# Kernel tuning notes

Hardware: AMD Instinct MI355X
Metric: run time of the kernel (lower is better)

## Reference

```python
import jax, jax.numpy as jnp
import numpy as np

B, S, D, H, E, K, V, FF, P = 1, 2048, 1024, 16, 8, 2, 32000, 4096, 4096
HD = D // H
EPS = 1e-5


def setup_inputs() -> dict:
    key = jax.random.key(0)
    ks = iter(jax.random.split(key, 64))
    w = lambda shape: jax.random.normal(next(ks), shape, jnp.float32) * 0.02
    d = {}
    d['input_ids'] = jax.random.randint(next(ks), (B, S), 0, V)
    d['embed_w'] = w((V, D))
    d['pos_w'] = w((P, D))
    for i in (0, 1):
        d[f'b{i}_ln1_g'] = jnp.ones(D); d[f'b{i}_ln1_b'] = jnp.zeros(D)
        d[f'b{i}_in_w'] = w((3 * D, D)); d[f'b{i}_in_b'] = jnp.zeros(3 * D)
        d[f'b{i}_out_w'] = w((D, D)); d[f'b{i}_out_b'] = jnp.zeros(D)
        d[f'b{i}_ln2_g'] = jnp.ones(D); d[f'b{i}_ln2_b'] = jnp.zeros(D)
    d['b0_ffn_w1'] = w((FF, D)); d['b0_ffn_b1'] = jnp.zeros(FF)
    d['b0_ffn_w2'] = w((D, FF)); d['b0_ffn_b2'] = jnp.zeros(D)
    d['b1_gate_w'] = w((E, D)); d['b1_gate_b'] = jnp.zeros(E)
    d['b1_moe_w1'] = w((E, FF, D)); d['b1_moe_b1'] = jnp.zeros((E, FF))
    d['b1_moe_w2'] = w((E, D, FF)); d['b1_moe_b2'] = jnp.zeros((E, D))
    d['norm_g'] = jnp.ones(D); d['norm_b'] = jnp.zeros(D)
    d['head_w'] = w((V, D))
    return d


def _ln(x, g, b):
    m = jnp.mean(x, -1, keepdims=True)
    v = jnp.mean(jnp.square(x - m), -1, keepdims=True)
    return (x - m) * jax.lax.rsqrt(v + EPS) * g + b


def _mha(x, in_w, in_b, out_w, out_b):
    # torch nn.MultiheadAttention (batch_first, eval mode -> no dropout)
    qkv = x @ in_w.T + in_b  # [B,S,3D]
    q, k, v = jnp.split(qkv, 3, axis=-1)
    q = q.reshape(B, S, H, HD); k = k.reshape(B, S, H, HD); v = v.reshape(B, S, H, HD)
    scores = jnp.einsum('bqhd,bkhd->bhqk', q, k) / jnp.sqrt(jnp.float32(HD))
    attn = jax.nn.softmax(scores, axis=-1)
    o = jnp.einsum('bhqk,bkhd->bqhd', attn, v).reshape(B, S, D)
    return o @ out_w.T + out_b


def _moe(h, gate_w, gate_b, w1, b1, w2, b2):
    scores = h @ gate_w.T + gate_b                       # [B,S,E]
    top_s, top_i = jax.lax.top_k(scores, K)              # [B,S,K]
    weights = jax.nn.softmax(top_s, axis=-1)             # softmax over top-k
    onehot = jax.nn.one_hot(top_i, E, dtype=h.dtype)     # [B,S,K,E]
    combine = jnp.sum(onehot * weights[..., None], axis=-2)  # [B,S,E]
    hid = jax.nn.gelu(jnp.einsum('bsd,efd->bsef', h, w1) + b1, approximate=False)
    eo = jnp.einsum('bsef,edf->bsed', hid, w2) + b2      # [B,S,E,D]
    return jnp.einsum('bsed,bse->bsd', eo, combine)


def reference(input_ids, embed_w, pos_w,
              b0_ln1_g, b0_ln1_b, b0_in_w, b0_in_b, b0_out_w, b0_out_b, b0_ln2_g, b0_ln2_b,
              b0_ffn_w1, b0_ffn_b1, b0_ffn_w2, b0_ffn_b2,
              b1_ln1_g, b1_ln1_b, b1_in_w, b1_in_b, b1_out_w, b1_out_b, b1_ln2_g, b1_ln2_b,
              b1_gate_w, b1_gate_b, b1_moe_w1, b1_moe_b1, b1_moe_w2, b1_moe_b2,
              norm_g, norm_b, head_w):
    pos = jnp.arange(S)[None, :]
    x = jnp.take(embed_w, input_ids, axis=0) + jnp.take(pos_w, pos, axis=0)
    # block 0: dense FFN
    x = x + _mha(_ln(x, b0_ln1_g, b0_ln1_b), b0_in_w, b0_in_b, b0_out_w, b0_out_b)
    h = _ln(x, b0_ln2_g, b0_ln2_b)
    ffn = jax.nn.gelu(h @ b0_ffn_w1.T + b0_ffn_b1, approximate=False) @ b0_ffn_w2.T + b0_ffn_b2
    x = x + ffn  # integration layer assumed residual add
    # block 1: MoE
    x = x + _mha(_ln(x, b1_ln1_g, b1_ln1_b), b1_in_w, b1_in_b, b1_out_w, b1_out_b)
    h = _ln(x, b1_ln2_g, b1_ln2_b)
    x = x + _moe(h, b1_gate_w, b1_gate_b, b1_moe_w1, b1_moe_b1, b1_moe_w2, b1_moe_b2)
    x = _ln(x, norm_g, norm_b)
    return x @ head_w.T
```

## Files before the change

kernel.cpp:

```cpp
#include <hip/hip_runtime.h>
#include <hip/hip_bf16.h>
#include <math.h>

typedef unsigned short ushort_t;
typedef __attribute__((ext_vector_type(8))) __bf16 bf16x8;
typedef __attribute__((ext_vector_type(4))) float f32x4;
typedef __attribute__((ext_vector_type(8))) short s8v;
typedef __attribute__((ext_vector_type(4))) short s4v;

#define SQ 2048
#define DM 1024
#define NH 16
#define HDIM 64
#define FFD 4096
#define NVOC 32000

__device__ inline float b2f(unsigned short u) {
  union { unsigned int i; float f; } x; x.i = ((unsigned int)u) << 16; return x.f;
}
__device__ inline unsigned short f2b(float f) {
  __hip_bfloat16 h = __float2bfloat16(f);
  return *reinterpret_cast<unsigned short*>(&h);
}
__device__ inline void split2(float x, ushort_t& h, ushort_t& l) {
  h = f2b(x);
  l = f2b(x - b2f(h));
}
__device__ inline float geluf(float v) {
  return 0.5f * v * (1.0f + erff(v * 0.70710678118654752f));
}
__device__ __forceinline__ void gld16(const void* g, void* l) {
  __builtin_amdgcn_global_load_lds(
      (const __attribute__((address_space(1))) void*)g,
      (__attribute__((address_space(3))) void*)l, 16, 0, 0);
}
#define MFMA __builtin_amdgcn_mfma_f32_16x16x32_bf16

template<int EPI, int NT, int KS>
__device__ __forceinline__ void gemmsp_body(
    const ushort_t* __restrict__ AH, const ushort_t* __restrict__ AL,
    int lda, long long bA,
    const ushort_t* __restrict__ BH, const ushort_t* __restrict__ BL,
    int ldb, long long bB,
    float* __restrict__ C, ushort_t* __restrict__ CH, ushort_t* __restrict__ CL,
    int ldc, long long bC, long long pC,
    int M, int N, int K, const float* __restrict__ bias, float alpha)
{
  int z = blockIdx.z, h = z / KS, kc = z % KS;
  const ushort_t* AHp = AH + (long long)h * bA + (long long)kc * K;
  const ushort_t* ALp = AL + (long long)h * bA + (long long)kc * K;
  const ushort_t* BHp = BH + (long long)h * bB + (long long)kc * K;
  const ushort_t* BLp = BL + (long long)h * bB + (long long)kc * K;
  int m0 = blockIdx.x * 128, n0 = blockIdx.y * NT;
  const int NF = NT / 32;

  __shared__ __align__(16) ushort_t sAH[128 * 32], sAL[128 * 32];
  __shared__ __align__(16) ushort_t sBH[NT * 32],  sBL[NT * 32];

  int tid = threadIdx.x, lane = tid & 63, wave = tid >> 6;
  int wr = (wave >> 1) * 64, wc = (wave & 1) * (NT >> 1);
  int l15 = lane & 15, l4 = lane >> 4;

  f32x4 acc[4][NF];
#pragma unroll
  for (int m = 0; m < 4; ++m)
#pragma unroll
    for (int n = 0; n < NF; ++n) acc[m][n] = (f32x4){0.f, 0.f, 0.f, 0.f};

  for (int k0 = 0; k0 < K; k0 += 32) {
#pragma unroll
    for (int i = 0; i < 2; ++i) {
      int fi = i * 2048 + tid * 8;
      int r = fi >> 5, chk = (fi >> 3) & 3;
      int scol = ((chk ^ ((r >> 1) & 3)) << 3);
      int ra = m0 + r; if (ra > M - 1) ra = M - 1;
      long long go = (long long)ra * lda + k0 + scol;
      gld16(AHp + go, &sAH[fi]);
      gld16(ALp + go, &sAL[fi]);
    }
#pragma unroll
    for (int i = 0; i < NT / 64; ++i) {
      int fi = i * 2048 + tid * 8;
      int r = fi >> 5, chk = (fi >> 3) & 3;
      int scol = ((chk ^ ((r >> 1) & 3)) << 3);
      int rb = n0 + r; if (rb > N - 1) rb = N - 1;
      long long go = (long long)rb * ldb + k0 + scol;
      gld16(BHp + go, &sBH[fi]);
      gld16(BLp + go, &sBL[fi]);
    }
    __syncthreads();
    bf16x8 ah[4], al[4], bh[NF], bl[NF];
#pragma unroll
    for (int m = 0; m < 4; ++m) {
      int r = wr + m * 16 + l15;
      int o = r * 32 + ((l4 ^ ((r >> 1) & 3)) << 3);
      ah[m] = *(const bf16x8*)&sAH[o];
      al[m] = *(const bf16x8*)&sAL[o];
    }
#pragma unroll
    for (int n = 0; n < NF; ++n) {
      int r = wc + n * 16 + l15;
      int o = r * 32 + ((l4 ^ ((r >> 1) & 3)) << 3);
      bh[n] = *(const bf16x8*)&sBH[o];
      bl[n] = *(const bf16x8*)&sBL[o];
    }
#pragma unroll
    for (int m = 0; m < 4; ++m)
#pragma unroll
      for (int n = 0; n < NF; ++n) {
        acc[m][n] = MFMA(ah[m], bh[n], acc[m][n], 0, 0, 0);
        acc[m][n] = MFMA(al[m], bh[n], acc[m][n], 0, 0, 0);
        acc[m][n] = MFMA(ah[m], bl[n], acc[m][n], 0, 0, 0);
      }
    __syncthreads();
  }

#pragma unroll
  for (int m = 0; m < 4; ++m) {
#pragma unroll
    for (int n = 0; n < NF; ++n) {
      int c = n0 + wc + n * 16 + l15;
      if (c >= N) continue;
      float bv = (EPI == 0 || EPI == 3 || EPI == 4) ? bias[c] : 0.f;
#pragma unroll
      for (int q = 0; q < 4; ++q) {
        int rr = m0 + wr + m * 16 + l4 * 4 + q;
        if (rr >= M) continue;
        float v = acc[m][n][q];
        if (EPI == 0) {
          ushort_t hh, ll; split2(v + bv, hh, ll);
          long long o = (long long)rr * ldc + c; CH[o] = hh; CL[o] = ll;
        } else if (EPI == 2) {
          C[(long long)kc * pC + (long long)rr * ldc + (long long)h * bC + c] = v;
        } else if (EPI == 3) {
          C[(long long)rr * ldc + c] += v + bv;
        } else if (EPI == 4) {
          ushort_t hh, ll; split2(geluf(v + bv), hh, ll);
          long long o = (long long)rr * ldc + c; CH[o] = hh; CL[o] = ll;
        }
      }
    }
  }
}

#define SP_ARGS const ushort_t* AH, const ushort_t* AL, int lda, long long bA, \
    const ushort_t* BH, const ushort_t* BL, int ldb, long long bB, \
    float* C, ushort_t* CH, ushort_t* CL, int ldc, long long bC, long long pC, \
    int M, int N, int K, const float* bias, float alpha
#define SP_PASS AH, AL, lda, bA, BH, BL, ldb, bB, C, CH, CL, ldc, bC, pC, M, N, K, bias, alpha

__global__ __launch_bounds__(256) void k_qkv (SP_ARGS) { gemmsp_body<0,128,1>(SP_PASS); }
__global__ __launch_bounds__(256) void k_outp(SP_ARGS) { gemmsp_body<2, 64,4>(SP_PASS); }
__global__ __launch_bounds__(256) void k_ffn1(SP_ARGS) { gemmsp_body<4,128,1>(SP_PASS); }
__global__ __launch_bounds__(256) void k_ffn2(SP_ARGS) { gemmsp_body<2, 64,2>(SP_PASS); }

template<int NP>
__global__ __launch_bounds__(256)
void reduce_add(float* __restrict__ x, const float* __restrict__ P, long long pC,
                const float* __restrict__ bias)
{
  int row = blockIdx.x, tid = threadIdx.x;
  long long o = (long long)row * DM + tid * 4;
  float4 xv = *(float4*)(x + o);
  float4 bv = *(const float4*)(bias + tid * 4);
  float sx = bv.x, sy = bv.y, sz = bv.z, sw = bv.w;
#pragma unroll
  for (int p = 0; p < NP; ++p) {
    float4 v = *(const float4*)(P + (long long)p * pC + o);
    sx += v.x; sy += v.y; sz += v.z; sw += v.w;
  }
  xv.x += sx; xv.y += sy; xv.z += sz; xv.w += sw;
  *(float4*)(x + o) = xv;
}

__global__ __launch_bounds__(256)
void k_attn(const ushort_t* __restrict__ qkvH, const ushort_t* __restrict__ qkvL,
            const ushort_t* __restrict__ VtH, const ushort_t* __restrict__ VtL,
            ushort_t* __restrict__ aH, ushort_t* __restrict__ aL)
{
  int f = blockIdx.x + blockIdx.y * gridDim.x;
  int logical = (f & 7) * 64 + (f >> 3);
  int q0 = (logical & 31) * 64;
  int h  = logical >> 5;

  __shared__ __align__(16) ushort_t sKH[4096], sKL[4096];
  __shared__ __align__(16) ushort_t sVH[4096], sVL[4096];
  __shared__ __align__(16) ushort_t sPH[4096], sPL[4096];

  int tid = threadIdx.x, lane = tid & 63, wave = tid >> 6;
  int l15 = lane & 15, l4 = lane >> 4;

  bf16x8 qh[2], ql[2];
  {
    long long base = (long long)(q0 + wave * 16 + l15) * (3 * DM) + h * 64 + l4 * 8;
    qh[0] = *(const bf16x8*)(qkvH + base);
    qh[1] = *(const bf16x8*)(qkvH + base + 32);
    ql[0] = *(const bf16x8*)(qkvL + base);
    ql[1] = *(const bf16x8*)(qkvL + base + 32);
  }

  float mrow[4], lrow[4];
  f32x4 Oacc[4];
#pragma unroll
  for (int r = 0; r < 4; ++r) { mrow[r] = -1e30f; lrow[r] = 0.f; }
#pragma unroll
  for (int n = 0; n < 4; ++n) Oacc[n] = (f32x4){0.f, 0.f, 0.f, 0.f};

  for (int kt = 0; kt < SQ / 64; ++kt) {
#pragma unroll
    for (int i = 0; i < 2; ++i) {
      int idx = i * 2048 + tid * 8;
      int row = idx >> 6, chk = (idx >> 3) & 7;
      int scol = ((chk ^ (row & 7)) << 3);
      long long gk = (long long)(kt * 64 + row) * (3 * DM) + DM + h * 64 + scol;
      long long gv = (long long)(h * 64 + row) * SQ + kt * 64 + scol;
      gld16(qkvH + gk, &sKH[idx]);
      gld16(qkvL + gk, &sKL[idx]);
      gld16(VtH + gv, &sVH[idx]);
      gld16(VtL + gv, &sVL[idx]);
    }
    __syncthreads();

    f32x4 S[4];
#pragma unroll
    for (int n = 0; n < 4; ++n) S[n] = (f32x4){0.f, 0.f, 0.f, 0.f};
#pragma unroll
    for (int kk = 0; kk < 64; kk += 32) {
      int kkI = kk >> 5;
      bf16x8 qhf = qh[kkI], qlf = ql[kkI];
#pragma unroll
      for (int n = 0; n < 4; ++n) {
        int br = n * 16 + l15;
        int bo = br * 64 + ((((kk >> 3) + l4) ^ (br & 7)) << 3);
        bf16x8 kh = *(const bf16x8*)&sKH[bo];
        bf16x8 kl = *(const bf16x8*)&sKL[bo];
        S[n] = MFMA(qhf, kh, S[n], 0, 0, 0);
        S[n] = MFMA(qlf, kh, S[n], 0, 0, 0);
        S[n] = MFMA(qhf, kl, S[n], 0, 0, 0);
      }
    }
    float tm[4], ts[4];
#pragma unroll
    for (int r = 0; r < 4; ++r) {
#pragma unroll
      for (int n = 0; n < 4; ++n) S[n][r] *= 0.125f;
      tm[r] = fmaxf(fmaxf(S[0][r], S[1][r]), fmaxf(S[2][r], S[3][r]));
    }
#pragma unroll
    for (int mk = 1; mk <= 8; mk <<= 1)
#pragma unroll
      for (int r = 0; r < 4; ++r) tm[r] = fmaxf(tm[r], __shfl_xor(tm[r], mk));
#pragma unroll
    for (int r = 0; r < 4; ++r) {
      float mn = fmaxf(mrow[r], tm[r]);
      float corr = __expf(mrow[r] - mn);
      mrow[r] = mn;
      float s = 0.f;
#pragma unroll
      for (int n = 0; n < 4; ++n) { S[n][r] = __expf(S[n][r] - mn); s += S[n][r]; }
      ts[r] = s;
      lrow[r] *= corr;
#pragma unroll
      for (int n = 0; n < 4; ++n) Oacc[n][r] *= corr;
    }
#pragma unroll
    for (int mk = 1; mk <= 8; mk <<= 1)
#pragma unroll
      for (int r = 0; r < 4; ++r) ts[r] += __shfl_xor(ts[r], mk);
#pragma unroll
    for (int r = 0; r < 4; ++r) lrow[r] += ts[r];

    {
      ushort_t* pH = &sPH[wave * 1024];
      ushort_t* pL = &sPL[wave * 1024];
#pragma unroll
      for (int n = 0; n < 4; ++n)
#pragma unroll
        for (int r = 0; r < 4; ++r) {
          int row = l4 * 4 + r, col = n * 16 + l15;
          int ad = row * 64 + (((col >> 3) ^ (row & 7)) << 3) + (col & 7);
          ushort_t hh, ll; split2(S[n][r], hh, ll);
          pH[ad] = hh; pL[ad] = ll;
        }
    }
    __syncthreads();
#pragma unroll
    for (int kk = 0; kk < 64; kk += 32) {
      int ao = wave * 1024 + l15 * 64 + ((((kk >> 3) + l4) ^ (l15 & 7)) << 3);
      bf16x8 ph = *(const bf16x8*)&sPH[ao];
      bf16x8 pl = *(const bf16x8*)&sPL[ao];
#pragma unroll
      for (int n = 0; n < 4; ++n) {
        int br = n * 16 + l15;
        int bo = br * 64 + ((((kk >> 3) + l4) ^ (br & 7)) << 3);
        bf16x8 vh = *(const bf16x8*)&sVH[bo];
        bf16x8 vl = *(const bf16x8*)&sVL[bo];
        Oacc[n] = MFMA(ph, vh, Oacc[n], 0, 0, 0);
        Oacc[n] = MFMA(pl, vh, Oacc[n], 0, 0, 0);
        Oacc[n] = MFMA(ph, vl, Oacc[n], 0, 0, 0);
      }
    }
    __syncthreads();
  }

#pragma unroll
  for (int n = 0; n < 4; ++n)
#pragma unroll
    for (int r = 0; r < 4; ++r) {
      int q = q0 + wave * 16 + l4 * 4 + r;
      int d = h * 64 + n * 16 + l15;
      float val = Oacc[n][r] / lrow[r];
      ushort_t hh, ll; split2(val, hh, ll);
      long long o = (long long)q * DM + d;
      aH[o] = hh; aL[o] = ll;
    }
}

template<int EPI, int BSRC, int SWAP, int KS, int XS>
__device__ __forceinline__ void gemm16_body(
    const ushort_t* __restrict__ A, int lda, long long bA,
    const void* __restrict__ Bv, int ldb, long long bB,
    void* __restrict__ Cv, int ldc, long long bC, long long pC,
    int M, int N, int K, const float* __restrict__ bias, int bBias,
    const int* __restrict__ offs)
{
  int bz = blockIdx.z;
  int z = bz / KS, kc = bz % KS;
  int Kc = K / KS;
  const ushort_t* Ap = A + (long long)z * bA + (long long)kc * Kc;
  int rowStart = 0, Meff = M;
  if (offs) { rowStart = offs[z]; Meff = offs[z + 1] - rowStart; }
  int bx = blockIdx.x, by = blockIdx.y;
  if (XS) {
    int flat = bx + by * gridDim.x;
    int cpx = (gridDim.x * gridDim.y) >> 3;
    int s = (flat & 7) * cpx + (flat >> 3);
    bx = s % gridDim.x; by = s / gridDim.x;
  }
  int m0 = (SWAP ? by : bx) * 128;
  if (m0 >= Meff) return;
  int n0 = (SWAP ? bx : by) * 128;

  __shared__ __align__(16) char smem[32768];
  ushort_t* As = (ushort_t*)smem;
  ushort_t* Bs = (ushort_t*)(smem + 16384);

  int tid = threadIdx.x, lane = tid & 63, wave = tid >> 6;
  int wr = (wave >> 1) * 64, wc = (wave & 1) * 64;
  int l15 = lane & 15, l4 = lane >> 4;

  f32x4 acc[4][4];
#pragma unroll
  for (int m = 0; m < 4; ++m)
#pragma unroll
    for (int n = 0; n < 4; ++n) acc[m][n] = (f32x4){0.f, 0.f, 0.f, 0.f};

  for (int k0 = 0; k0 < Kc; k0 += 64) {
#pragma unroll
    for (int i = 0; i < 4; ++i) {
      int idx = i * 2048 + tid * 8;
      int row = idx >> 6, chk = (idx >> 3) & 7;
      int scol = ((chk ^ (row & 7)) << 3);
      int ra = m0 + row; if (ra > Meff - 1) ra = Meff - 1;
      gld16(Ap + (long long)(rowStart + ra) * lda + k0 + scol, &As[idx]);
    }
    if (BSRC == 1) {
      const ushort_t* Bp = (const ushort_t*)Bv + (long long)z * bB + (long long)kc * Kc;
#pragma unroll
      for (int i = 0; i < 4; ++i) {
        int idx = i * 2048 + tid * 8;
        int row = idx >> 6, chk = (idx >> 3) & 7;
        int scol = ((chk ^ (row & 7)) << 3);
        int rb = n0 + row; if (rb > N - 1) rb = N - 1;
        gld16(Bp + (long long)rb * ldb + k0 + scol, &Bs[idx]);
      }
    } else {
      const float* Bf = (const float*)Bv + (long long)z * bB + (long long)kc * Kc;
#pragma unroll
      for (int i = 0; i < 8; ++i) {
        int g = tid + i * 256;
        int r = g >> 4, c4 = (g & 15) * 4;
        int rb = n0 + r; if (rb > N - 1) rb = N - 1;
        float4 fv = *(const float4*)(Bf + (long long)rb * ldb + k0 + c4);
        s4v o; o[0] = (short)f2b(fv.x); o[1] = (short)f2b(fv.y);
        o[2] = (short)f2b(fv.z); o[3] = (short)f2b(fv.w);
        int dst = r * 64 + (((c4 >> 3) ^ (r & 7)) << 3) + (c4 & 7);
        *(s4v*)&Bs[dst] = o;
      }
    }
    __syncthreads();
#pragma unroll
    for (int kk = 0; kk < 64; kk += 32) {
      bf16x8 af[4], bfr[4];
#pragma unroll
      for (int m = 0; m < 4; ++m) {
        int r = wr + m * 16 + l15;
        af[m] = *(const bf16x8*)&As[r * 64 + ((((kk >> 3) + l4) ^ (r & 7)) << 3)];
      }
#pragma unroll
      for (int n = 0; n < 4; ++n) {
        int r = wc + n * 16 + l15;
        bfr[n] = *(const bf16x8*)&Bs[r * 64 + ((((kk >> 3) + l4) ^ (r & 7)) << 3)];
      }
#pragma unroll
      for (int m = 0; m < 4; ++m)
#pragma unroll
        for (int n = 0; n < 4; ++n)
          acc[m][n] = MFMA(af[m], bfr[n], acc[m][n], 0, 0, 0);
    }
    __syncthreads();
  }

  if (EPI == 6 || EPI == 7) {
    float* fE = (float*)smem;
#pragma unroll
    for (int h2 = 0; h2 < 2; ++h2) {
      if ((wave >> 1) == h2) {
#pragma unroll
        for (int m = 0; m < 4; ++m)
#pragma unroll
          for (int n = 0; n < 4; ++n)
#pragma unroll
            for (int q = 0; q < 4; ++q)
              fE[(m * 16 + l4 * 4 + q) * 128 + wc + n * 16 + l15] = acc[m][n][q];
      }
      __syncthreads();
#pragma unroll
      for (int i = 0; i < 8; ++i) {
        int lin = tid + i * 256;
        int row = lin >> 5, c4 = (lin & 31) << 2;
        int gr = m0 + h2 * 64 + row;
        if (gr < Meff) {
          f32x4 v4 = *(const f32x4*)&fE[row * 128 + c4];
          long long crow = rowStart + gr;
          float* dst = (float*)Cv + (EPI == 7 ? (long long)kc * pC : 0LL)
                       + crow * ldc + n0 + c4;
          if (EPI == 6) __builtin_nontemporal_store(v4, (f32x4*)dst);
          else          *(f32x4*)dst = v4;
        }
      }
      __syncthreads();
    }
    return;
  }

#pragma unroll
  for (int m = 0; m < 4; ++m) {
#pragma unroll
    for (int n = 0; n < 4; ++n) {
      int c = n0 + wc + n * 16 + l15;
      if (c >= N) continue;
      float bv = (EPI == 2) ? bias[(long long)z * bBias + c] : 0.f;
#pragma unroll
      for (int q = 0; q < 4; ++q) {
        int rr = m0 + wr + m * 16 + l4 * 4 + q;
        if (rr >= Meff) continue;
        float v = acc[m][n][q];
        long long crow = rowStart + rr;
        if (EPI == 2)
          ((ushort_t*)Cv)[crow * ldc + (long long)z * bC + c] = f2b(geluf(v + bv));
      }
    }
  }
}

#define G16_ARGS const ushort_t* A, int lda, long long bA, const void* Bv, \
    int ldb, long long bB, void* Cv, int ldc, long long bC, long long pC, \
    int M, int N, int K, const float* bias, int bBias, const int* offs
#define G16_PASS A, lda, bA, Bv, ldb, bB, Cv, ldc, bC, pC, M, N, K, bias, bBias, offs

__global__ __launch_bounds__(256) void k_moe1   (G16_ARGS) { gemm16_body<2,1,1,1,0>(G16_PASS); }
__global__ __launch_bounds__(256) void k_moe2   (G16_ARGS) { gemm16_body<7,1,1,2,0>(G16_PASS); }
__global__ __launch_bounds__(256) void k_head_bf(G16_ARGS) { gemm16_body<6,1,0,1,1>(G16_PASS); }
__global__ __launch_bounds__(256) void k_head_f (G16_ARGS) { gemm16_body<6,0,0,1,1>(G16_PASS); }

__global__ __launch_bounds__(256)
void cvt_split2(const float* __restrict__ s0, ushort_t* __restrict__ dh0,
                ushort_t* __restrict__ dl0,
                const float* __restrict__ s1, ushort_t* __restrict__ dh1,
                ushort_t* __restrict__ dl1, int n4)
{
  const float* s = blockIdx.y ? s1 : s0;
  ushort_t* dh = blockIdx.y ? dh1 : dh0;
  ushort_t* dl = blockIdx.y ? dl1 : dl0;
  int i = blockIdx.x * blockDim.x + threadIdx.x;
  int stride = gridDim.x * blockDim.x;
  for (; i < n4; i += stride) {
    float4 f = ((const float4*)s)[i];
    s4v h, l; ushort_t hh, ll;
    split2(f.x, hh, ll); h[0] = (short)hh; l[0] = (short)ll;
    split2(f.y, hh, ll); h[1] = (short)hh; l[1] = (short)ll;
    split2(f.z, hh, ll); h[2] = (short)hh; l[2] = (short)ll;
    split2(f.w, hh, ll); h[3] = (short)hh; l[3] = (short)ll;
    ((s4v*)dh)[i] = h; ((s4v*)dl)[i] = l;
  }
}

__global__ __launch_bounds__(256)
void cvt_bf16(const float* __restrict__ s, ushort_t* __restrict__ d, int n4)
{
  int i = blockIdx.x * blockDim.x + threadIdx.x;
  int stride = gridDim.x * blockDim.x;
  for (; i < n4; i += stride) {
    float4 f = ((const float4*)s)[i];
    s4v o; o[0] = (short)f2b(f.x); o[1] = (short)f2b(f.y);
    o[2] = (short)f2b(f.z); o[3] = (short)f2b(f.w);
    ((s4v*)d)[i] = o;
  }
}

__global__ __launch_bounds__(256)
void embed_kernel(const int* __restrict__ ids, const float* __restrict__ ew,
                  const float* __restrict__ pw, float* __restrict__ x,
                  int* __restrict__ counts)
{
  int srow = blockIdx.x, tid = threadIdx.x;
  if (srow == 0 && tid < 8) counts[tid] = 0;
  int id = ids[srow];
  const float4 e = *(const float4*)(ew + (long long)id * DM + tid * 4);
  const float4 p = *(const float4*)(pw + (long long)srow * DM + tid * 4);
  float4* xr = (float4*)(x + (long long)srow * DM) + tid;
  *xr = make_float4(e.x + p.x, e.y + p.y, e.z + p.z, e.w + p.w);
}

template<int MODE>
__global__ __launch_bounds__(256)
void ln_kernel(const float* __restrict__ x, const float* __restrict__ g,
               const float* __restrict__ b, ushort_t* __restrict__ outH,
               ushort_t* __restrict__ outL)
{
  int row = blockIdx.x, tid = threadIdx.x;
  float4 v = ((const float4*)(x + (long long)row * DM))[tid];
  __shared__ float sm1[4], sm2[4];
  float s = v.x + v.y + v.z + v.w;
  for (int o = 32; o > 0; o >>= 1) s += __shfl_down(s, o);
  if ((tid & 63) == 0) sm1[tid >> 6] = s;
  __syncthreads();
  float mean = (sm1[0] + sm1[1] + sm1[2] + sm1[3]) * (1.0f / DM);
  float d0 = v.x - mean, d1 = v.y - mean, d2 = v.z - mean, d3 = v.w - mean;
  float q = d0 * d0 + d1 * d1 + d2 * d2 + d3 * d3;
  for (int o = 32; o > 0; o >>= 1) q += __shfl_down(q, o);
  if ((tid & 63) == 0) sm2[tid >> 6] = q;
  __syncthreads();
  float var = (sm2[0] + sm2[1] + sm2[2] + sm2[3]) * (1.0f / DM);
  float rstd = rsqrtf(var + 1e-5f);
  float4 gv = ((const float4*)g)[tid];
  float4 bv = ((const float4*)b)[tid];
  float o0 = d0 * rstd * gv.x + bv.x, o1 = d1 * rstd * gv.y + bv.y;
  float o2 = d2 * rstd * gv.z + bv.z, o3 = d3 * rstd * gv.w + bv.w;
  long long base = (long long)row * DM + tid * 4;
  if (MODE == 0) {
    ushort_t hh, ll;
    split2(o0, hh, ll); outH[base + 0] = hh; outL[base + 0] = ll;
    split2(o1, hh, ll); outH[base + 1] = hh; outL[base + 1] = ll;
    split2(o2, hh, ll); outH[base + 2] = hh; outL[base + 2] = ll;
    split2(o3, hh, ll); outH[base + 3] = hh; outL[base + 3] = ll;
  } else {
    outH[base + 0] = f2b(o0); outH[base + 1] = f2b(o1);
    outH[base + 2] = f2b(o2); outH[base + 3] = f2b(o3);
  }
}

__global__ __launch_bounds__(256)
void transpose_v2(const ushort_t* __restrict__ qH, const ushort_t* __restrict__ qL,
                  ushort_t* __restrict__ vH, ushort_t* __restrict__ vL)
{
  __shared__ ushort_t tH[64][65], tL[64][65];
  int j0 = blockIdx.x * 64, h = blockIdx.y;
  int tid = threadIdx.x;
  int jr = tid >> 2, d0 = (tid & 3) * 16;
  long long so = (long long)(j0 + jr) * (3 * DM) + 2 * DM + h * 64 + d0;
#pragma unroll
  for (int i = 0; i < 16; ++i) { tH[jr][d0 + i] = qH[so + i]; tL[jr][d0 + i] = qL[so + i]; }
  __syncthreads();
  int dd = tid >> 2, jc = (tid & 3) * 16;
  long long dofs = (long long)(h * 64 + dd) * SQ + j0 + jc;
#pragma unroll
  for (int i = 0; i < 16; ++i) { vH[dofs + i] = tH[jc + i][dd]; vL[dofs + i] = tL[jc + i][dd]; }
}

__global__ __launch_bounds__(256)
void ln_gate_top2(const float* __restrict__ x, const float* __restrict__ g,
                  const float* __restrict__ b, const float* __restrict__ gw,
                  const float* __restrict__ gb, int* __restrict__ topi,
                  float* __restrict__ topw, int* __restrict__ counts,
                  ushort_t* __restrict__ outH)
{
  int row = blockIdx.x, tid = threadIdx.x;
  float4 v = ((const float4*)(x + (long long)row * DM))[tid];
  __shared__ float sm1[4], sm2[4];
  __shared__ float se[8][4];
  float s = v.x + v.y + v.z + v.w;
  for (int o = 32; o > 0; o >>= 1) s += __shfl_down(s, o);
  if ((tid & 63) == 0) sm1[tid >> 6] = s;
  __syncthreads();
  float mean = (sm1[0] + sm1[1] + sm1[2] + sm1[3]) * (1.0f / DM);
  float d0 = v.x - mean, d1 = v.y - mean, d2 = v.z - mean, d3 = v.w - mean;
  float q = d0 * d0 + d1 * d1 + d2 * d2 + d3 * d3;
  for (int o = 32; o > 0; o >>= 1) q += __shfl_down(q, o);
  if ((tid & 63) == 0) sm2[tid >> 6] = q;
  __syncthreads();
  float var = (sm2[0] + sm2[1] + sm2[2] + sm2[3]) * (1.0f / DM);
  float rstd = rsqrtf(var + 1e-5f);
  float4 gv = ((const float4*)g)[tid];
  float4 bv = ((const float4*)b)[tid];
  float h0 = d0 * rstd * gv.x + bv.x, h1 = d1 * rstd * gv.y + bv.y;
  float h2 = d2 * rstd * gv.z + bv.z, h3 = d3 * rstd * gv.w + bv.w;
  long long base = (long long)row * DM + tid * 4;
  outH[base + 0] = f2b(h0); outH[base + 1] = f2b(h1);
  outH[base + 2] = f2b(h2); outH[base + 3] = f2b(h3);
#pragma unroll
  for (int e = 0; e < 8; ++e) {
    float4 w = ((const float4*)(gw + (long long)e * DM))[tid];
    float p = h0 * w.x + h1 * w.y + h2 * w.z + h3 * w.w;
    for (int o = 32; o > 0; o >>= 1) p += __shfl_down(p, o);
    if ((tid & 63) == 0) se[e][tid >> 6] = p;
  }
  __syncthreads();
  if (tid == 0) {
    float sc[8];
#pragma unroll
    for (int e = 0; e < 8; ++e)
      sc[e] = se[e][0] + se[e][1] + se[e][2] + se[e][3] + gb[e];
    int i1 = 0; float m1 = sc[0];
    for (int e = 1; e < 8; ++e) if (sc[e] > m1) { m1 = sc[e]; i1 = e; }
    int i2 = -1; float m2 = -1e30f;
    for (int e = 0; e < 8; ++e) if (e != i1 && sc[e] > m2) { m2 = sc[e]; i2 = e; }
    float e2 = __expf(m2 - m1);
    float w1 = 1.f / (1.f + e2);
    topi[row * 2] = i1; topi[row * 2 + 1] = i2;
    topw[row * 2] = w1; topw[row * 2 + 1] = 1.f - w1;
    atomicAdd(&counts[i1], 1);
    atomicAdd(&counts[i2], 1);
  }
}

__global__ void moe_prefix(const int* __restrict__ counts, int* __restrict__ offs,
                           int* __restrict__ cursors)
{
  if (threadIdx.x == 0 && blockIdx.x == 0) {
    int a = 0;
    for (int e = 0; e < 8; ++e) { offs[e] = a; a += counts[e]; cursors[e] = 0; }
    offs[8] = a;
  }
}

__global__ __launch_bounds__(256)
void moe_gather(const ushort_t* __restrict__ hH, const int* __restrict__ topi,
                const float* __restrict__ topw, const int* __restrict__ offs,
                int* __restrict__ cursors, int* __restrict__ tokIdx,
                float* __restrict__ tokW, int* __restrict__ slotOf,
                ushort_t* __restrict__ Xg)
{
  int tok = blockIdx.x, tid = threadIdx.x;
  __shared__ int s0s, s1s;
  if (tid == 0) {
    int e0 = topi[tok * 2], e1 = topi[tok * 2 + 1];
    int s0 = offs[e0] + atomicAdd(&cursors[e0], 1);
    int s1 = offs[e1] + atomicAdd(&cursors[e1], 1);
    tokIdx[s0] = tok; tokW[s0] = topw[tok * 2];
    tokIdx[s1] = tok; tokW[s1] = topw[tok * 2 + 1];
    slotOf[tok * 2] = s0; slotOf[tok * 2 + 1] = s1;
    s0s = s0; s1s = s1;
  }
  __syncthreads();
  s4v v = ((const s4v*)(hH + (long long)tok * DM))[tid];
  ((s4v*)(Xg + (long long)s0s * DM))[tid] = v;
  ((s4v*)(Xg + (long long)s1s * DM))[tid] = v;
}

__global__ __launch_bounds__(256)
void moe_reduce(float* __restrict__ x, const float* __restrict__ eo, long long pC,
                const int* __restrict__ slotOf, const int* __restrict__ topi,
                const float* __restrict__ topw, const float* __restrict__ b2)
{
  int tok = blockIdx.x, tid = threadIdx.x;
  int s0 = slotOf[tok * 2], s1 = slotOf[tok * 2 + 1];
  int e0 = topi[tok * 2], e1 = topi[tok * 2 + 1];
  float w0 = topw[tok * 2], w1 = topw[tok * 2 + 1];
  float4 a  = ((const float4*)(eo + (long long)s0 * DM))[tid];
  float4 a2 = ((const float4*)(eo + pC + (long long)s0 * DM))[tid];
  float4 b  = ((const float4*)(eo + (long long)s1 * DM))[tid];
  float4 b2v= ((const float4*)(eo + pC + (long long)s1 * DM))[tid];
  float4 ba = ((const float4*)(b2 + (long long)e0 * DM))[tid];
  float4 bb = ((const float4*)(b2 + (long long)e1 * DM))[tid];
  float4* xr = (float4*)(x + (long long)tok * DM) + tid;
  float4 xv = *xr;
  xv.x += w0 * (a.x + a2.x + ba.x) + w1 * (b.x + b2v.x + bb.x);
  xv.y += w0 * (a.y + a2.y + ba.y) + w1 * (b.y + b2v.y + bb.y);
  xv.z += w0 * (a.z + a2.z + ba.z) + w1 * (b.z + b2v.z + bb.z);
  xv.w += w0 * (a.w + a2.w + ba.w) + w1 * (b.w + b2v.w + bb.w);
  *xr = xv;
}

extern "C" void kernel_launch(void* const* d_in, const int* in_sizes, int n_in,
                              void* d_out, int out_size, void* d_ws, size_t ws_size,
                              hipStream_t stream)
{
  const int* ids = (const int*)d_in[0];
  const float* embed_w = (const float*)d_in[1];
  const float* pos_w   = (const float*)d_in[2];
  const float* ln1_g[2] = {(const float*)d_in[3],  (const float*)d_in[11]};
  const float* ln1_b[2] = {(const float*)d_in[4],  (const float*)d_in[12]};
  const float* in_w[2]  = {(const float*)d_in[5],  (const float*)d_in[13]};
  const float* in_b[2]  = {(const float*)d_in[6],  (const float*)d_in[14]};
  const float* out_w[2] = {(const float*)d_in[7],  (const float*)d_in[15]};
  const float* out_b[2] = {(const float*)d_in[8],  (const float*)d_in[16]};
  const float* ln2_g[2] = {(const float*)d_in[9],  (const float*)d_in[17]};
  const float* ln2_b[2] = {(const float*)d_in[10], (const float*)d_in[18]};
  const float* ffn_w1 = (const float*)d_in[19];
  const float* ffn_b1 = (const float*)d_in[20];
  const float* ffn_w2 = (const float*)d_in[21];
  const float* ffn_b2 = (const float*)d_in[22];
  const float* gate_w = (const float*)d_in[23];
  const float* gate_b = (const float*)d_in[24];
  const float* moe_w1 = (const float*)d_in[25];
  const float* moe_b1 = (const float*)d_in[26];
  const float* moe_w2 = (const float*)d_in[27];
  const float* moe_b2 = (const float*)d_in[28];
  const float* norm_g = (const float*)d_in[29];
  const float* norm_b = (const float*)d_in[30];
  const float* head_w = (const float*)d_in[31];

  char* ob = (char*)d_out;
  size_t off = 0;
  auto alloc = [&](size_t bytes) {
    char* p = ob + off;
    off = (off + bytes + 255) & ~(size_t)255;
    return p;
  };
  float*    x      = (float*)alloc((size_t)SQ * DM * 4);
  ushort_t* hbufH  = (ushort_t*)alloc((size_t)SQ * DM * 2);
  ushort_t* hbufL  = (ushort_t*)alloc((size_t)SQ * DM * 2);
  ushort_t* qkvH   = (ushort_t*)alloc((size_t)SQ * 3 * DM * 2);
  ushort_t* qkvL   = (ushort_t*)alloc((size_t)SQ * 3 * DM * 2);
  ushort_t* VtH    = (ushort_t*)alloc((size_t)NH * HDIM * SQ * 2);
  ushort_t* VtL    = (ushort_t*)alloc((size_t)NH * HDIM * SQ * 2);
  char*     resv   = (char*)alloc((size_t)32 << 20);
  ushort_t* attnH  = (ushort_t*)alloc((size_t)SQ * DM * 2);
  ushort_t* attnL  = (ushort_t*)alloc((size_t)SQ * DM * 2);
  ushort_t* Xg     = (ushort_t*)alloc((size_t)2 * SQ * DM * 2);
  int*      topi   = (int*)alloc(SQ * 2 * 4);
  float*    topw   = (float*)alloc(SQ * 2 * 4);
  int*      tokIdx = (int*)alloc(2 * SQ * 4);
  float*    tokW   = (float*)alloc(2 * SQ * 4);
  int*      slotOf = (int*)alloc(2 * SQ * 4);
  int*      counts = (int*)alloc(256);
  int*      offsb  = (int*)alloc(256);
  int*      cursors= (int*)alloc(256);
  ushort_t* ffnH   = (ushort_t*)alloc((size_t)SQ * FFD * 2);
  ushort_t* ffnL   = (ushort_t*)alloc((size_t)SQ * FFD * 2);
  float*    eo     = (float*)alloc((size_t)2 * 2 * SQ * DM * 4);
  ushort_t* inwH[2], *inwL[2], *outwH[2], *outwL[2];
  ushort_t* wsplit0 = (ushort_t*)alloc(0);
  inwH[0]  = (ushort_t*)alloc((size_t)3 * DM * DM * 2);
  inwL[0]  = (ushort_t*)alloc((size_t)3 * DM * DM * 2);
  inwH[1]  = (ushort_t*)alloc((size_t)3 * DM * DM * 2);
  inwL[1]  = (ushort_t*)alloc((size_t)3 * DM * DM * 2);
  outwH[0] = (ushort_t*)alloc((size_t)DM * DM * 2);
  outwL[0] = (ushort_t*)alloc((size_t)DM * DM * 2);
  outwH[1] = (ushort_t*)alloc((size_t)DM * DM * 2);
  outwL[1] = (ushort_t*)alloc((size_t)DM * DM * 2);
  ushort_t* f1H = (ushort_t*)alloc((size_t)FFD * DM * 2);
  ushort_t* f1L = (ushort_t*)alloc((size_t)FFD * DM * 2);
  ushort_t* f2H = (ushort_t*)alloc((size_t)DM * FFD * 2);
  ushort_t* f2L = (ushort_t*)alloc((size_t)DM * FFD * 2);
  ushort_t* moe_w1b = wsplit0;
  ushort_t* moe_w2b = qkvH;
  ushort_t* moehid  = ffnH;
  float*    pp      = eo;
  const long long eoPC = (long long)2 * SQ * DM;
  const long long ppPC = (long long)SQ * DM;
  ushort_t* hfin    = (ushort_t*)d_ws;
  bool wsBig = ws_size >= ((size_t)70 << 20);
  ushort_t* head_wb = (ushort_t*)((char*)d_ws + ((size_t)4 << 20));
  (void)resv;

  embed_kernel<<<SQ, 256, 0, stream>>>(ids, embed_w, pos_w, x, counts);
  cvt_split2<<<dim3(512, 2), 256, 0, stream>>>(
      in_w[0], inwH[0], inwL[0], in_w[1], inwH[1], inwL[1], 3 * DM * DM / 4);
  cvt_split2<<<dim3(512, 2), 256, 0, stream>>>(
      out_w[0], outwH[0], outwL[0], out_w[1], outwH[1], outwL[1], DM * DM / 4);
  cvt_split2<<<dim3(512, 2), 256, 0, stream>>>(
      ffn_w1, f1H, f1L, ffn_w2, f2H, f2L, FFD * DM / 4);
  if (wsBig)
    cvt_bf16<<<1024, 256, 0, stream>>>(head_w, head_wb, NVOC * DM / 4);

  for (int L = 0; L < 2; ++L) {
    ln_kernel<0><<<SQ, 256, 0, stream>>>(x, ln1_g[L], ln1_b[L], hbufH, hbufL);
    k_qkv<<<dim3(16, 24, 1), 256, 0, stream>>>(
        hbufH, hbufL, DM, 0, inwH[L], inwL[L], DM, 0,
        nullptr, qkvH, qkvL, 3 * DM, 0, 0,
        SQ, 3 * DM, DM, in_b[L], 1.f);
    transpose_v2<<<dim3(SQ / 64, NH), 256, 0, stream>>>(qkvH, qkvL, VtH, VtL);
    k_attn<<<dim3(SQ / 64, NH), 256, 0, stream>>>(qkvH, qkvL, VtH, VtL,
                                                  attnH, attnL);
    k_outp<<<dim3(16, 16, 4), 256, 0, stream>>>(
        attnH, attnL, DM, 0, outwH[L], outwL[L], DM, 0,
        pp, nullptr, nullptr, DM, 0, ppPC,
        SQ, DM, DM / 4, nullptr, 1.f);
    reduce_add<4><<<SQ, 256, 0, stream>>>(x, pp, ppPC, out_b[L]);
    if (L == 0) {
      ln_kernel<0><<<SQ, 256, 0, stream>>>(x, ln2_g[0], ln2_b[0], hbufH, hbufL);
      k_ffn1<<<dim3(16, 32, 1), 256, 0, stream>>>(
          hbufH, hbufL, DM, 0, f1H, f1L, DM, 0,
          nullptr, ffnH, ffnL, FFD, 0, 0,
          SQ, FFD, DM, ffn_b1, 1.f);
      k_ffn2<<<dim3(16, 16, 2), 256, 0, stream>>>(
          ffnH, ffnL, FFD, 0, f2H, f2L, FFD, 0,
          pp, nullptr, nullptr, DM, 0, ppPC,
          SQ, DM, FFD / 2, nullptr, 1.f);
      reduce_add<2><<<SQ, 256, 0, stream>>>(x, pp, ppPC, ffn_b2);
    } else {
      cvt_bf16<<<2048, 256, 0, stream>>>(moe_w1, moe_w1b, 8 * FFD * DM / 4);
      cvt_bf16<<<2048, 256, 0, stream>>>(moe_w2, moe_w2b, 8 * DM * FFD / 4);
      ln_gate_top2<<<SQ, 256, 0, stream>>>(x, ln2_g[1], ln2_b[1], gate_w, gate_b,
                                           topi, topw, counts, hbufH);
      moe_prefix<<<1, 64, 0, stream>>>(counts, offsb, cursors);
      moe_gather<<<SQ, 256, 0, stream>>>(hbufH, topi, topw, offsb, cursors,
                                         tokIdx, tokW, slotOf, Xg);
      k_moe1<<<dim3(32, 16, 8), 256, 0, stream>>>(
          Xg, DM, 0, moe_w1b, DM, (long long)FFD * DM,
          moehid, FFD, 0, 0, SQ, FFD, DM, moe_b1, FFD, offsb);
      k_moe2<<<dim3(8, 16, 16), 256, 0, stream>>>(
          moehid, FFD, 0, moe_w2b, FFD, (long long)DM * FFD,
          eo, DM, 0, eoPC, SQ, DM, FFD, nullptr, 0, offsb);
      moe_reduce<<<SQ, 256, 0, stream>>>(x, eo, eoPC, slotOf, topi, topw, moe_b2);
    }
  }
  ln_kernel<1><<<SQ, 256, 0, stream>>>(x, norm_g, norm_b, hfin, nullptr);
  if (wsBig)
    k_head_bf<<<dim3(16, 250, 1), 256, 0, stream>>>(
        hfin, DM, 0, head_wb, DM, 0, d_out, NVOC, 0, 0,
        SQ, NVOC, DM, nullptr, 0, nullptr);
  else
    k_head_f<<<dim3(16, 250, 1), 256, 0, stream>>>(
        hfin, DM, 0, head_w, DM, 0, d_out, NVOC, 0, 0,
        SQ, NVOC, DM, nullptr, 0, nullptr);
}
```

Baseline: 1.235 ms.

## Fuse residual reductions into LayerNorm kernels and V transpose into QKV epilogue

Removes the separate reduce_add kernels by folding the split-K partial-sum reduction and bias add into the following LayerNorm (and gate/top-2) kernels. The QKV GEMM now writes the V slice directly in transposed layout from its epilogue, so the transpose_v2 kernel is gone. The MoE combine is fused with the final LayerNorm. This cuts several launches and full passes over the activation buffer. The V columns of the QKV output are no longer written row-major, and the transposed stores are short strided vectors.

Result: no change. 1.216 ms (-1.6%).

```diff
diff --git a/kernel.cpp b/kernel.cpp
--- a/kernel.cpp
+++ b/kernel.cpp
@@ -44,7 +44,8 @@
     int ldb, long long bB,
     float* __restrict__ C, ushort_t* __restrict__ CH, ushort_t* __restrict__ CL,
     int ldc, long long bC, long long pC,
-    int M, int N, int K, const float* __restrict__ bias, float alpha)
+    int M, int N, int K, const float* __restrict__ bias, float alpha,
+    ushort_t* __restrict__ TH, ushort_t* __restrict__ TL)
 {
   int z = blockIdx.z, h = z / KS, kc = z % KS;
   const ushort_t* AHp = AH + (long long)h * bA + (long long)kc * K;
@@ -115,25 +116,45 @@
     __syncthreads();
   }
 
+  if (EPI == 5 && n0 >= 2 * DM) {
+#pragma unroll
+    for (int m = 0; m < 4; ++m) {
+      int rbase = m0 + wr + m * 16 + l4 * 4;
+#pragma unroll
+      for (int n = 0; n < NF; ++n) {
+        int c = n0 + wc + n * 16 + l15;
+        int d = c - 2 * DM;
+        float bv = bias[c];
+        s4v hv, lv;
+#pragma unroll
+        for (int q = 0; q < 4; ++q) {
+          ushort_t hh, ll; split2(acc[m][n][q] + bv, hh, ll);
+          hv[q] = (short)hh; lv[q] = (short)ll;
+        }
+        *(s4v*)&TH[(long long)d * SQ + rbase] = hv;
+        *(s4v*)&TL[(long long)d * SQ + rbase] = lv;
+      }
+    }
+    return;
+  }
+
 #pragma unroll
   for (int m = 0; m < 4; ++m) {
 #pragma unroll
     for (int n = 0; n < NF; ++n) {
       int c = n0 + wc + n * 16 + l15;
       if (c >= N) continue;
-      float bv = (EPI == 0 || EPI == 3 || EPI == 4) ? bias[c] : 0.f;
+      float bv = (EPI == 4 || EPI == 5) ? bias[c] : 0.f;
 #pragma unroll
       for (int q = 0; q < 4; ++q) {
         int rr = m0 + wr + m * 16 + l4 * 4 + q;
         if (rr >= M) continue;
         float v = acc[m][n][q];
-        if (EPI == 0) {
+        if (EPI == 5) {
           ushort_t hh, ll; split2(v + bv, hh, ll);
           long long o = (long long)rr * ldc + c; CH[o] = hh; CL[o] = ll;
         } else if (EPI == 2) {
           C[(long long)kc * pC + (long long)rr * ldc + (long long)h * bC + c] = v;
-        } else if (EPI == 3) {
-          C[(long long)rr * ldc + c] += v + bv;
         } else if (EPI == 4) {
           ushort_t hh, ll; split2(geluf(v + bv), hh, ll);
           long long o = (long long)rr * ldc + c; CH[o] = hh; CL[o] = ll;
@@ -146,32 +167,14 @@
 #define SP_ARGS const ushort_t* AH, const ushort_t* AL, int lda, long long bA, \
     const ushort_t* BH, const ushort_t* BL, int ldb, long long bB, \
     float* C, ushort_t* CH, ushort_t* CL, int ldc, long long bC, long long pC, \
-    int M, int N, int K, const float* bias, float alpha
-#define SP_PASS AH, AL, lda, bA, BH, BL, ldb, bB, C, CH, CL, ldc, bC, pC, M, N, K, bias, alpha
-
-__global__ __launch_bounds__(256) void k_qkv (SP_ARGS) { gemmsp_body<0,128,1>(SP_PASS); }
+    int M, int N, int K, const float* bias, float alpha, \
+    ushort_t* TH, ushort_t* TL
+#define SP_PASS AH, AL, lda, bA, BH, BL, ldb, bB, C, CH, CL, ldc, bC, pC, M, N, K, bias, alpha, TH, TL
+
+__global__ __launch_bounds__(256) void k_qkv (SP_ARGS) { gemmsp_body<5,128,1>(SP_PASS); }
 __global__ __launch_bounds__(256) void k_outp(SP_ARGS) { gemmsp_body<2, 64,4>(SP_PASS); }
 __global__ __launch_bounds__(256) void k_ffn1(SP_ARGS) { gemmsp_body<4,128,1>(SP_PASS); }
 __global__ __launch_bounds__(256) void k_ffn2(SP_ARGS) { gemmsp_body<2, 64,2>(SP_PASS); }
-
-template<int NP>
-__global__ __launch_bounds__(256)
-void reduce_add(float* __restrict__ x, const float* __restrict__ P, long long pC,
-                const float* __restrict__ bias)
-{
-  int row = blockIdx.x, tid = threadIdx.x;
-  long long o = (long long)row * DM + tid * 4;
-  float4 xv = *(float4*)(x + o);
-  float4 bv = *(const float4*)(bias + tid * 4);
-  float sx = bv.x, sy = bv.y, sz = bv.z, sw = bv.w;
-#pragma unroll
-  for (int p = 0; p < NP; ++p) {
-    float4 v = *(const float4*)(P + (long long)p * pC + o);
-    sx += v.x; sy += v.y; sz += v.z; sw += v.w;
-  }
-  xv.x += sx; xv.y += sy; xv.z += sz; xv.w += sw;
-  *(float4*)(x + o) = xv;
-}
 
 __global__ __launch_bounds__(256)
 void k_attn(const ushort_t* __restrict__ qkvH, const ushort_t* __restrict__ qkvL,
@@ -523,14 +526,27 @@
   *xr = make_float4(e.x + p.x, e.y + p.y, e.z + p.z, e.w + p.w);
 }
 
-template<int MODE>
+template<int MODE, int NP>
 __global__ __launch_bounds__(256)
-void ln_kernel(const float* __restrict__ x, const float* __restrict__ g,
-               const float* __restrict__ b, ushort_t* __restrict__ outH,
-               ushort_t* __restrict__ outL)
+void ln_fused(float* __restrict__ x, const float* __restrict__ P, long long pC,
+              const float* __restrict__ bias_pre,
+              const float* __restrict__ g, const float* __restrict__ b,
+              ushort_t* __restrict__ outH, ushort_t* __restrict__ outL)
 {
   int row = blockIdx.x, tid = threadIdx.x;
-  float4 v = ((const float4*)(x + (long long)row * DM))[tid];
+  long long xo = (long long)row * DM + tid * 4;
+  float4 v = *(const float4*)(x + xo);
+  if (NP > 0) {
+    float4 bp = *(const float4*)(bias_pre + tid * 4);
+    float sx = bp.x, sy = bp.y, sz = bp.z, sw = bp.w;
+#pragma unroll
+    for (int p = 0; p < NP; ++p) {
+      float4 pv = *(const float4*)(P + (long long)p * pC + xo);
+      sx += pv.x; sy += pv.y; sz += pv.z; sw += pv.w;
+    }
+    v.x += sx; v.y += sy; v.z += sz; v.w += sw;
+    *(float4*)(x + xo) = v;
+  }
   __shared__ float sm1[4], sm2[4];
   float s = v.x + v.y + v.z + v.w;
   for (int o = 32; o > 0; o >>= 1) s += __shfl_down(s, o);
@@ -562,32 +578,27 @@
 }
 
 __global__ __launch_bounds__(256)
-void transpose_v2(const ushort_t* __restrict__ qH, const ushort_t* __restrict__ qL,
-                  ushort_t* __restrict__ vH, ushort_t* __restrict__ vL)
-{
-  __shared__ ushort_t tH[64][65], tL[64][65];
-  int j0 = blockIdx.x * 64, h = blockIdx.y;
-  int tid = threadIdx.x;
-  int jr = tid >> 2, d0 = (tid & 3) * 16;
-  long long so = (long long)(j0 + jr) * (3 * DM) + 2 * DM + h * 64 + d0;
-#pragma unroll
-  for (int i = 0; i < 16; ++i) { tH[jr][d0 + i] = qH[so + i]; tL[jr][d0 + i] = qL[so + i]; }
-  __syncthreads();
-  int dd = tid >> 2, jc = (tid & 3) * 16;
-  long long dofs = (long long)(h * 64 + dd) * SQ + j0 + jc;
-#pragma unroll
-  for (int i = 0; i < 16; ++i) { vH[dofs + i] = tH[jc + i][dd]; vL[dofs + i] = tL[jc + i][dd]; }
-}
-
-__global__ __launch_bounds__(256)
-void ln_gate_top2(const float* __restrict__ x, const float* __restrict__ g,
-                  const float* __restrict__ b, const float* __restrict__ gw,
-                  const float* __restrict__ gb, int* __restrict__ topi,
-                  float* __restrict__ topw, int* __restrict__ counts,
-                  ushort_t* __restrict__ outH)
+void ln_gate_top2(float* __restrict__ x, const float* __restrict__ P,
+                  long long pC, const float* __restrict__ bias_pre,
+                  const float* __restrict__ g, const float* __restrict__ b,
+                  const float* __restrict__ gw, const float* __restrict__ gb,
+                  int* __restrict__ topi, float* __restrict__ topw,
+                  int* __restrict__ counts, ushort_t* __restrict__ outH)
 {
   int row = blockIdx.x, tid = threadIdx.x;
-  float4 v = ((const float4*)(x + (long long)row * DM))[tid];
+  long long xo = (long long)row * DM + tid * 4;
+  float4 v = *(const float4*)(x + xo);
+  {
+    float4 bp = *(const float4*)(bias_pre + tid * 4);
+    float sx = bp.x, sy = bp.y, sz = bp.z, sw = bp.w;
+#pragma unroll
+    for (int p = 0; p < 4; ++p) {
+      float4 pv = *(const float4*)(P + (long long)p * pC + xo);
+      sx += pv.x; sy += pv.y; sz += pv.z; sw += pv.w;
+    }
+    v.x += sx; v.y += sy; v.z += sz; v.w += sw;
+    *(float4*)(x + xo) = v;
+  }
   __shared__ float sm1[4], sm2[4];
   __shared__ float se[8][4];
   float s = v.x + v.y + v.z + v.w;
@@ -670,9 +681,11 @@
 }
 
 __global__ __launch_bounds__(256)
-void moe_reduce(float* __restrict__ x, const float* __restrict__ eo, long long pC,
-                const int* __restrict__ slotOf, const int* __restrict__ topi,
-                const float* __restrict__ topw, const float* __restrict__ b2)
+void moe_ln_final(const float* __restrict__ x, const float* __restrict__ eo,
+                  long long pC, const int* __restrict__ slotOf,
+                  const int* __restrict__ topi, const float* __restrict__ topw,
+                  const float* __restrict__ b2, const float* __restrict__ g,
+                  const float* __restrict__ b, ushort_t* __restrict__ outH)
 {
   int tok = blockIdx.x, tid = threadIdx.x;
   int s0 = slotOf[tok * 2], s1 = slotOf[tok * 2 + 1];
@@ -680,17 +693,35 @@
   float w0 = topw[tok * 2], w1 = topw[tok * 2 + 1];
   float4 a  = ((const float4*)(eo + (long long)s0 * DM))[tid];
   float4 a2 = ((const float4*)(eo + pC + (long long)s0 * DM))[tid];
-  float4 b  = ((const float4*)(eo + (long long)s1 * DM))[tid];
-  float4 b2v= ((const float4*)(eo + pC + (long long)s1 * DM))[tid];
+  float4 bb1= ((const float4*)(eo + (long long)s1 * DM))[tid];
+  float4 bb2= ((const float4*)(eo + pC + (long long)s1 * DM))[tid];
   float4 ba = ((const float4*)(b2 + (long long)e0 * DM))[tid];
-  float4 bb = ((const float4*)(b2 + (long long)e1 * DM))[tid];
-  float4* xr = (float4*)(x + (long long)tok * DM) + tid;
-  float4 xv = *xr;
-  xv.x += w0 * (a.x + a2.x + ba.x) + w1 * (b.x + b2v.x + bb.x);
-  xv.y += w0 * (a.y + a2.y + ba.y) + w1 * (b.y + b2v.y + bb.y);
-  xv.z += w0 * (a.z + a2.z + ba.z) + w1 * (b.z + b2v.z + bb.z);
-  xv.w += w0 * (a.w + a2.w + ba.w) + w1 * (b.w + b2v.w + bb.w);
-  *xr = xv;
+  float4 bbb= ((const float4*)(b2 + (long long)e1 * DM))[tid];
+  float4 v = ((const float4*)(x + (long long)tok * DM))[tid];
+  v.x += w0 * (a.x + a2.x + ba.x) + w1 * (bb1.x + bb2.x + bbb.x);
+  v.y += w0 * (a.y + a2.y + ba.y) + w1 * (bb1.y + bb2.y + bbb.y);
+  v.z += w0 * (a.z + a2.z + ba.z) + w1 * (bb1.z + bb2.z + bbb.z);
+  v.w += w0 * (a.w + a2.w + ba.w) + w1 * (bb1.w + bb2.w + bbb.w);
+  __shared__ float sm1[4], sm2[4];
+  float s = v.x + v.y + v.z + v.w;
+  for (int o = 32; o > 0; o >>= 1) s += __shfl_down(s, o);
+  if ((tid & 63) == 0) sm1[tid >> 6] = s;
+  __syncthreads();
+  float mean = (sm1[0] + sm1[1] + sm1[2] + sm1[3]) * (1.0f / DM);
+  float d0 = v.x - mean, d1 = v.y - mean, d2 = v.z - mean, d3 = v.w - mean;
+  float q = d0 * d0 + d1 * d1 + d2 * d2 + d3 * d3;
+  for (int o = 32; o > 0; o >>= 1) q += __shfl_down(q, o);
+  if ((tid & 63) == 0) sm2[tid >> 6] = q;
+  __syncthreads();
+  float var = (sm2[0] + sm2[1] + sm2[2] + sm2[3]) * (1.0f / DM);
+  float rstd = rsqrtf(var + 1e-5f);
+  float4 gv = ((const float4*)g)[tid];
+  float4 bv = ((const float4*)b)[tid];
+  long long base = (long long)tok * DM + tid * 4;
+  outH[base + 0] = f2b(d0 * rstd * gv.x + bv.x);
+  outH[base + 1] = f2b(d1 * rstd * gv.y + bv.y);
+  outH[base + 2] = f2b(d2 * rstd * gv.z + bv.z);
+  outH[base + 3] = f2b(d3 * rstd * gv.w + bv.w);
 }
 
 extern "C" void kernel_launch(void* const* d_in, const int* in_sizes, int n_in,
@@ -786,49 +817,56 @@
   if (wsBig)
     cvt_bf16<<<1024, 256, 0, stream>>>(head_w, head_wb, NVOC * DM / 4);
 
-  for (int L = 0; L < 2; ++L) {
-    ln_kernel<0><<<SQ, 256, 0, stream>>>(x, ln1_g[L], ln1_b[L], hbufH, hbufL);
-    k_qkv<<<dim3(16, 24, 1), 256, 0, stream>>>(
-        hbufH, hbufL, DM, 0, inwH[L], inwL[L], DM, 0,
-        nullptr, qkvH, qkvL, 3 * DM, 0, 0,
-        SQ, 3 * DM, DM, in_b[L], 1.f);
-    transpose_v2<<<dim3(SQ / 64, NH), 256, 0, stream>>>(qkvH, qkvL, VtH, VtL);
-    k_attn<<<dim3(SQ / 64, NH), 256, 0, stream>>>(qkvH, qkvL, VtH, VtL,
-                                                  attnH, attnL);
-    k_outp<<<dim3(16, 16, 4), 256, 0, stream>>>(
-        attnH, attnL, DM, 0, outwH[L], outwL[L], DM, 0,
-        pp, nullptr, nullptr, DM, 0, ppPC,
-        SQ, DM, DM / 4, nullptr, 1.f);
-    reduce_add<4><<<SQ, 256, 0, stream>>>(x, pp, ppPC, out_b[L]);
-    if (L == 0) {
-      ln_kernel<0><<<SQ, 256, 0, stream>>>(x, ln2_g[0], ln2_b[0], hbufH, hbufL);
-      k_ffn1<<<dim3(16, 32, 1), 256, 0, stream>>>(
-          hbufH, hbufL, DM, 0, f1H, f1L, DM, 0,
-          nullptr, ffnH, ffnL, FFD, 0, 0,
-          SQ, FFD, DM, ffn_b1, 1.f);
-      k_ffn2<<<dim3(16, 16, 2), 256, 0, stream>>>(
-          ffnH, ffnL, FFD, 0, f2H, f2L, FFD, 0,
-          pp, nullptr, nullptr, DM, 0, ppPC,
-          SQ, DM, FFD / 2, nullptr, 1.f);
-      reduce_add<2><<<SQ, 256, 0, stream>>>(x, pp, ppPC, ffn_b2);
-    } else {
-      cvt_bf16<<<2048, 256, 0, stream>>>(moe_w1, moe_w1b, 8 * FFD * DM / 4);
-      cvt_bf16<<<2048, 256, 0, stream>>>(moe_w2, moe_w2b, 8 * DM * FFD / 4);
-      ln_gate_top2<<<SQ, 256, 0, stream>>>(x, ln2_g[1], ln2_b[1], gate_w, gate_b,
-                                           topi, topw, counts, hbufH);
-      moe_prefix<<<1, 64, 0, stream>>>(counts, offsb, cursors);
-      moe_gather<<<SQ, 256, 0, stream>>>(hbufH, topi, topw, offsb, cursors,
-                                         tokIdx, tokW, slotOf, Xg);
-      k_moe1<<<dim3(32, 16, 8), 256, 0, stream>>>(
-          Xg, DM, 0, moe_w1b, DM, (long long)FFD * DM,
-          moehid, FFD, 0, 0, SQ, FFD, DM, moe_b1, FFD, offsb);
-      k_moe2<<<dim3(8, 16, 16), 256, 0, stream>>>(
-          moehid, FFD, 0, moe_w2b, FFD, (long long)DM * FFD,
-          eo, DM, 0, eoPC, SQ, DM, FFD, nullptr, 0, offsb);
-      moe_reduce<<<SQ, 256, 0, stream>>>(x, eo, eoPC, slotOf, topi, topw, moe_b2);
-    }
-  }
-  ln_kernel<1><<<SQ, 256, 0, stream>>>(x, norm_g, norm_b, hfin, nullptr);
+  ln_fused<0, 0><<<SQ, 256, 0, stream>>>(x, nullptr, 0, nullptr,
+                                         ln1_g[0], ln1_b[0], hbufH, hbufL);
+  k_qkv<<<dim3(16, 24, 1), 256, 0, stream>>>(
+      hbufH, hbufL, DM, 0, inwH[0], inwL[0], DM, 0,
+      nullptr, qkvH, qkvL, 3 * DM, 0, 0,
+      SQ, 3 * DM, DM, in_b[0], 1.f, VtH, VtL);
+  k_attn<<<dim3(SQ / 64, NH), 256, 0, stream>>>(qkvH, qkvL, VtH, VtL,
+                                                attnH, attnL);
+  k_outp<<<dim3(16, 16, 4), 256, 0, stream>>>(
+      attnH, attnL, DM, 0, outwH[0], outwL[0], DM, 0,
+      pp, nullptr, nullptr, DM, 0, ppPC,
+      SQ, DM, DM / 4, nullptr, 1.f, nullptr, nullptr);
+  ln_fused<0, 4><<<SQ, 256, 0, stream>>>(x, pp, ppPC, out_b[0],
+                                         ln2_g[0], ln2_b[0], hbufH, hbufL);
+  k_ffn1<<<dim3(16, 32, 1), 256, 0, stream>>>(
+      hbufH, hbufL, DM, 0, f1H, f1L, DM, 0,
+      nullptr, ffnH, ffnL, FFD, 0, 0,
+      SQ, FFD, DM, ffn_b1, 1.f, nullptr, nullptr);
+  k_ffn2<<<dim3(16, 16, 2), 256, 0, stream>>>(
+      ffnH, ffnL, FFD, 0, f2H, f2L, FFD, 0,
+      pp, nullptr, nullptr, DM, 0, ppPC,
+      SQ, DM, FFD / 2, nullptr, 1.f, nullptr, nullptr);
+  ln_fused<0, 2><<<SQ, 256, 0, stream>>>(x, pp, ppPC, ffn_b2,
+                                         ln1_g[1], ln1_b[1], hbufH, hbufL);
+  k_qkv<<<dim3(16, 24, 1), 256, 0, stream>>>(
+      hbufH, hbufL, DM, 0, inwH[1], inwL[1], DM, 0,
+      nullptr, qkvH, qkvL, 3 * DM, 0, 0,
+      SQ, 3 * DM, DM, in_b[1], 1.f, VtH, VtL);
+  k_attn<<<dim3(SQ / 64, NH), 256, 0, stream>>>(qkvH, qkvL, VtH, VtL,
+                                                attnH, attnL);
+  k_outp<<<dim3(16, 16, 4), 256, 0, stream>>>(
+      attnH, attnL, DM, 0, outwH[1], outwL[1], DM, 0,
+      pp, nullptr, nullptr, DM, 0, ppPC,
+      SQ, DM, DM / 4, nullptr, 1.f, nullptr, nullptr);
+  cvt_bf16<<<2048, 256, 0, stream>>>(moe_w1, moe_w1b, 8 * FFD * DM / 4);
+  cvt_bf16<<<2048, 256, 0, stream>>>(moe_w2, moe_w2b, 8 * DM * FFD / 4);
+  ln_gate_top2<<<SQ, 256, 0, stream>>>(x, pp, ppPC, out_b[1],
+                                       ln2_g[1], ln2_b[1], gate_w, gate_b,
+                                       topi, topw, counts, hbufH);
+  moe_prefix<<<1, 64, 0, stream>>>(counts, offsb, cursors);
+  moe_gather<<<SQ, 256, 0, stream>>>(hbufH, topi, topw, offsb, cursors,
+                                     tokIdx, tokW, slotOf, Xg);
+  k_moe1<<<dim3(32, 16, 8), 256, 0, stream>>>(
+      Xg, DM, 0, moe_w1b, DM, (long long)FFD * DM,
+      moehid, FFD, 0, 0, SQ, FFD, DM, moe_b1, FFD, offsb);
+  k_moe2<<<dim3(8, 16, 16), 256, 0, stream>>>(
+      moehid, FFD, 0, moe_w2b, FFD, (long long)DM * FFD,
+      eo, DM, 0, eoPC, SQ, DM, FFD, nullptr, 0, offsb);
+  moe_ln_final<<<SQ, 256, 0, stream>>>(x, eo, eoPC, slotOf, topi, topw,
+                                       moe_b2, norm_g, norm_b, hfin);
   if (wsBig)
     k_head_bf<<<dim3(16, 250, 1), 256, 0, stream>>>(
         hfin, DM, 0, head_wb, DM, 0, d_out, NVOC, 0, 0,
```
